# Performance work log

Measured on AMD Instinct MI355X. Metric: run time of the kernel, lower is better.

The kernel has to match this reference:

```python
import jax, jax.numpy as jnp
import numpy as np
import math

B, N, D = 4, 16384, 256
M, H = 64, 8
HD = D // H

def setup_inputs() -> dict:
    key = jax.random.key(0)
    ks = jax.random.split(key, 5)
    s = 1.0 / math.sqrt(D)
    return {
        "x": jax.random.normal(ks[0], (B, N, D), dtype=jnp.float32),
        "Ws": jax.random.normal(ks[1], (M, D), dtype=jnp.float32) * s,
        "bs": jnp.zeros((M,), dtype=jnp.float32),
        "Wqkv": jax.random.normal(ks[2], (3 * D, D), dtype=jnp.float32) * s,
        "Wo": jax.random.normal(ks[3], (D, D), dtype=jnp.float32) * s,
        "bo": jnp.zeros((D,), dtype=jnp.float32),
    }

def reference(x, Ws, bs, Wqkv, Wo, bo):
    # slice weights: softmax over N (dim=1), matching the torch code exactly
    logits = jnp.einsum('bnd,md->bnm', x, Ws) + bs          # [B,N,M]
    weights = jax.nn.softmax(logits, axis=1)                # softmax over N
    # pooling: tokens[b,m,d] = sum_n w[b,n,m] * x[b,n,d]
    tokens = jnp.einsum('bnm,bnd->bmd', weights, x)         # [B,M,D]
    # qkv projection (no bias)
    qkv = jnp.einsum('bmd,ed->bme', tokens, Wqkv)           # [B,M,3D]
    qkv = qkv.reshape(B, M, 3, H, HD)
    q = qkv[:, :, 0].transpose(0, 2, 1, 3)                  # [B,H,M,HD]
    k = qkv[:, :, 1].transpose(0, 2, 1, 3)
    v = qkv[:, :, 2].transpose(0, 2, 1, 3)
    scale = 1.0 / math.sqrt(HD)
    attn = jax.nn.softmax(jnp.einsum('bhmd,bhkd->bhmk', q, k) * scale, axis=-1)
    token_out = jnp.einsum('bhmk,bhkd->bhmd', attn, v)      # [B,H,M,HD]
    token_out = token_out.transpose(0, 2, 1, 3).reshape(B, M, D)
    token_out = jnp.einsum('bmd,ed->bme', token_out, Wo) + bo
    # unpooling: out[b,n,d] = sum_m w[b,n,m] * token_out[b,m,d]
    out = jnp.einsum('bnm,bmd->bnd', weights, token_out)    # [B,N,D]
    return out
```

## Files before the change

### kernel.cpp

```cpp
#include <hip/hip_runtime.h>
#include <math.h>

constexpr int B = 4;
constexpr int N = 16384;
constexpr int D = 256;
constexpr int M = 64;
constexpr int H = 8;

typedef __attribute__((ext_vector_type(8))) short short8;
typedef __attribute__((ext_vector_type(4))) float floatx4;

__device__ __forceinline__ float4 ld4(const float* p) {
  return *reinterpret_cast<const float4*>(p);
}
__device__ __forceinline__ void st4(float* p, float a, float b, float c, float d) {
  *reinterpret_cast<float4*>(p) = make_float4(a, b, c, d);
}
__device__ __forceinline__ unsigned short f2bf(float f) {
  unsigned u = __float_as_uint(f);
  unsigned r = (u + 0x7fffu + ((u >> 16) & 1u)) >> 16;
  return (unsigned short)r;
}

#define FMA16(acc, a4, b4)                       \
  do {                                           \
    acc[0][0] = fmaf(a4.x, b4.x, acc[0][0]);     \
    acc[0][1] = fmaf(a4.x, b4.y, acc[0][1]);     \
    acc[0][2] = fmaf(a4.x, b4.z, acc[0][2]);     \
    acc[0][3] = fmaf(a4.x, b4.w, acc[0][3]);     \
    acc[1][0] = fmaf(a4.y, b4.x, acc[1][0]);     \
    acc[1][1] = fmaf(a4.y, b4.y, acc[1][1]);     \
    acc[1][2] = fmaf(a4.y, b4.z, acc[1][2]);     \
    acc[1][3] = fmaf(a4.y, b4.w, acc[1][3]);     \
    acc[2][0] = fmaf(a4.z, b4.x, acc[2][0]);     \
    acc[2][1] = fmaf(a4.z, b4.y, acc[2][1]);     \
    acc[2][2] = fmaf(a4.z, b4.z, acc[2][2]);     \
    acc[2][3] = fmaf(a4.z, b4.w, acc[2][3]);     \
    acc[3][0] = fmaf(a4.w, b4.x, acc[3][0]);     \
    acc[3][1] = fmaf(a4.w, b4.y, acc[3][1]);     \
    acc[3][2] = fmaf(a4.w, b4.z, acc[3][2]);     \
    acc[3][3] = fmaf(a4.w, b4.w, acc[3][3]);     \
  } while (0)

__global__ __launch_bounds__(256) void k1_fused(
    const float* __restrict__ x, const float* __restrict__ Ws,
    const float* __restrict__ bs, unsigned short* __restrict__ xbT,
    unsigned short* __restrict__ En, unsigned short* __restrict__ Et,
    float* __restrict__ denom) {
  __shared__ unsigned short Xt[64][264];
  __shared__ unsigned short Wt[64][264];
  __shared__ unsigned short Es[64][72];
  __shared__ float red[64];
  const int b = blockIdx.y;
  const int n0 = blockIdx.x * 64;
  const int tid = threadIdx.x;
  const int w = tid >> 6, l = tid & 63;

#pragma unroll
  for (int p = 0; p < 16; ++p) {
    const int i = p * 256 + tid;
    const int row = i >> 6;
    const int c4 = (i & 63) * 4;
    float4 v = ld4(&x[((size_t)(b * N + n0 + row)) * D + c4]);
    unsigned u0 = (unsigned)f2bf(v.x) | ((unsigned)f2bf(v.y) << 16);
    unsigned u1 = (unsigned)f2bf(v.z) | ((unsigned)f2bf(v.w) << 16);
    *reinterpret_cast<uint2*>(&Xt[row][c4]) = make_uint2(u0, u1);
    float4 wv = ld4(&Ws[(size_t)row * D + c4]);
    unsigned w0 = (unsigned)f2bf(wv.x) | ((unsigned)f2bf(wv.y) << 16);
    unsigned w1 = (unsigned)f2bf(wv.z) | ((unsigned)f2bf(wv.w) << 16);
    *reinterpret_cast<uint2*>(&Wt[row][c4]) = make_uint2(w0, w1);
  }
  if (tid < 64) red[tid] = 0.0f;
  __syncthreads();

  floatx4 acc[4] = {{0.f, 0.f, 0.f, 0.f},
                    {0.f, 0.f, 0.f, 0.f},
                    {0.f, 0.f, 0.f, 0.f},
                    {0.f, 0.f, 0.f, 0.f}};
  const int ar = w * 16 + (l & 15);
  const int q8 = (l >> 4) * 8;
#pragma unroll
  for (int ks = 0; ks < 8; ++ks) {
    short8 a = *reinterpret_cast<short8*>(&Xt[ar][ks * 32 + q8]);
#pragma unroll
    for (int mt = 0; mt < 4; ++mt) {
      short8 bf = *reinterpret_cast<short8*>(&Wt[mt * 16 + (l & 15)][ks * 32 + q8]);
      acc[mt] = __builtin_amdgcn_mfma_f32_16x16x32_bf16(a, bf, acc[mt], 0, 0, 0);
    }
  }

  {
    const int t = tid;
#pragma unroll
    for (int g = 0; g < 4; ++g) {
      unsigned dw[8];
#pragma unroll
      for (int j = 0; j < 8; ++j) {
        const unsigned lo = Xt[g * 16 + 2 * j][t];
        const unsigned hi = Xt[g * 16 + 2 * j + 1][t];
        dw[j] = lo | (hi << 16);
      }
      const size_t base = ((size_t)(b * D + t)) * N + n0 + g * 16;
      *reinterpret_cast<uint4*>(&xbT[base]) =
          make_uint4(dw[0], dw[1], dw[2], dw[3]);
      *reinterpret_cast<uint4*>(&xbT[base + 8]) =
          make_uint4(dw[4], dw[5], dw[6], dw[7]);
    }
  }

#pragma unroll
  for (int mt = 0; mt < 4; ++mt) {
    const int m = mt * 16 + (l & 15);
    const float bsm = bs[m];
    float s = 0.0f;
#pragma unroll
    for (int r = 0; r < 4; ++r) {
      const int n = w * 16 + (l >> 4) * 4 + r;
      const float e = expf(acc[mt][r] + bsm);
      s += e;
      Es[n][m] = f2bf(e);
    }
    atomicAdd(&red[m], s);
  }
  __syncthreads();
  if (tid < 64) atomicAdd(&denom[b * M + tid], red[tid]);
#pragma unroll
  for (int p = 0; p < 2; ++p) {
    const int g = p * 256 + tid;
    const int n = g >> 3;
    const int m0 = (g & 7) * 8;
    short8 v = *reinterpret_cast<short8*>(&Es[n][m0]);
    *reinterpret_cast<short8*>(&En[((size_t)(b * N + n0 + n)) * M + m0]) = v;
  }
#pragma unroll
  for (int p = 0; p < 2; ++p) {
    const int g = p * 256 + tid;
    const int m = g >> 3;
    const int n8 = (g & 7) * 8;
    unsigned short bu[8];
#pragma unroll
    for (int k = 0; k < 8; ++k) bu[k] = Es[n8 + k][m];
    uint4 pk;
    pk.x = (unsigned)bu[0] | ((unsigned)bu[1] << 16);
    pk.y = (unsigned)bu[2] | ((unsigned)bu[3] << 16);
    pk.z = (unsigned)bu[4] | ((unsigned)bu[5] << 16);
    pk.w = (unsigned)bu[6] | ((unsigned)bu[7] << 16);
    *reinterpret_cast<uint4*>(&Et[((size_t)(b * M + m)) * N + n0 + n8]) = pk;
  }
}

__global__ __launch_bounds__(256) void k2_pool(
    const unsigned short* __restrict__ Et, const unsigned short* __restrict__ xbT,
    float* __restrict__ tokens) {
  __shared__ unsigned short EtS[64][72];
  __shared__ unsigned short XtS[64][72];
  const int dt = blockIdx.x, nc = blockIdx.y, b = blockIdx.z;
  const int d0 = dt * 64;
  const int tid = threadIdx.x;
  const int w = tid >> 6, l = tid & 63;
  floatx4 acc[4] = {{0.f, 0.f, 0.f, 0.f},
                    {0.f, 0.f, 0.f, 0.f},
                    {0.f, 0.f, 0.f, 0.f},
                    {0.f, 0.f, 0.f, 0.f}};
  const int q8 = (l >> 4) * 8;
  for (int kc = 0; kc < 8; ++kc) {
    const int nb = nc * 512 + kc * 64;
    __syncthreads();
#pragma unroll
    for (int p = 0; p < 2; ++p) {
      const int g = p * 256 + tid;
      const int row = g >> 3;
      const int c8 = (g & 7) * 8;
      *reinterpret_cast<short8*>(&EtS[row][c8]) =
          *reinterpret_cast<const short8*>(
              &Et[((size_t)(b * M + row)) * N + nb + c8]);
      *reinterpret_cast<short8*>(&XtS[row][c8]) =
          *reinterpret_cast<const short8*>(
              &xbT[((size_t)(b * D + d0 + row)) * N + nb + c8]);
    }
    __syncthreads();
#pragma unroll
    for (int ks = 0; ks < 2; ++ks) {
      short8 a = *reinterpret_cast<short8*>(&EtS[w * 16 + (l & 15)][ks * 32 + q8]);
#pragma unroll
      for (int dtile = 0; dtile < 4; ++dtile) {
        short8 bf = *reinterpret_cast<short8*>(
            &XtS[dtile * 16 + (l & 15)][ks * 32 + q8]);
        acc[dtile] =
            __builtin_amdgcn_mfma_f32_16x16x32_bf16(a, bf, acc[dtile], 0, 0, 0);
      }
    }
  }
#pragma unroll
  for (int dtile = 0; dtile < 4; ++dtile)
#pragma unroll
    for (int r = 0; r < 4; ++r) {
      const int m = w * 16 + (l >> 4) * 4 + r;
      const int d = d0 + dtile * 16 + (l & 15);
      atomicAdd(&tokens[((size_t)(b * M + m)) * D + d], acc[dtile][r]);
    }
}

__global__ __launch_bounds__(256) void k_proj(
    const float* __restrict__ A, const float* __restrict__ W,
    const float* __restrict__ bias, const float* __restrict__ denom,
    float* __restrict__ OutF, unsigned short* __restrict__ OutT, const int EC,
    const int mode) {
  __shared__ unsigned short At[64][264];
  __shared__ unsigned short Wt[64][264];
  __shared__ float Cs[64][68];
  const int et = blockIdx.x;
  const int b = blockIdx.y;
  const int tid = threadIdx.x;
  const int w = tid >> 6, l = tid & 63;
#pragma unroll
  for (int p = 0; p < 16; ++p) {
    const int i = p * 256 + tid;
    const int row = i >> 6;
    const int c4 = (i & 63) * 4;
    float4 av = ld4(&A[((size_t)(b * M + row)) * D + c4]);
    unsigned a0 = (unsigned)f2bf(av.x) | ((unsigned)f2bf(av.y) << 16);
    unsigned a1 = (unsigned)f2bf(av.z) | ((unsigned)f2bf(av.w) << 16);
    *reinterpret_cast<uint2*>(&At[row][c4]) = make_uint2(a0, a1);
    float4 wv = ld4(&W[((size_t)(et * 64 + row)) * D + c4]);
    unsigned w0 = (unsigned)f2bf(wv.x) | ((unsigned)f2bf(wv.y) << 16);
    unsigned w1 = (unsigned)f2bf(wv.z) | ((unsigned)f2bf(wv.w) << 16);
    *reinterpret_cast<uint2*>(&Wt[row][c4]) = make_uint2(w0, w1);
  }
  __syncthreads();
  floatx4 acc[4] = {{0.f, 0.f, 0.f, 0.f},
                    {0.f, 0.f, 0.f, 0.f},
                    {0.f, 0.f, 0.f, 0.f},
                    {0.f, 0.f, 0.f, 0.f}};
  const int ar = w * 16 + (l & 15);
  const int q8 = (l >> 4) * 8;
#pragma unroll
  for (int ks = 0; ks < 8; ++ks) {
    short8 a = *reinterpret_cast<short8*>(&At[ar][ks * 32 + q8]);
#pragma unroll
    for (int mt = 0; mt < 4; ++mt) {
      short8 bf = *reinterpret_cast<short8*>(&Wt[mt * 16 + (l & 15)][ks * 32 + q8]);
      acc[mt] = __builtin_amdgcn_mfma_f32_16x16x32_bf16(a, bf, acc[mt], 0, 0, 0);
    }
  }
  if (mode == 0) {
#pragma unroll
    for (int mt = 0; mt < 4; ++mt) {
#pragma unroll
      for (int r = 0; r < 4; ++r) {
        const int row = w * 16 + (l >> 4) * 4 + r;
        const float rcp = 1.0f / denom[b * M + row];
        const int e = et * 64 + mt * 16 + (l & 15);
        OutF[((size_t)(b * M + row)) * EC + e] = acc[mt][r] * rcp;
      }
    }
  } else {
#pragma unroll
    for (int mt = 0; mt < 4; ++mt) {
#pragma unroll
      for (int r = 0; r < 4; ++r) {
        const int row = w * 16 + (l >> 4) * 4 + r;
        const float rcp = 1.0f / denom[b * M + row];
        const int el = mt * 16 + (l & 15);
        const float bv = bias[et * 64 + el];
        Cs[row][el] = (acc[mt][r] + bv) * rcp;
      }
    }
    __syncthreads();
#pragma unroll
    for (int p = 0; p < 2; ++p) {
      const int g = p * 256 + tid;
      const int e = g >> 3;
      const int m0 = (g & 7) * 8;
      unsigned short bu[8];
#pragma unroll
      for (int k = 0; k < 8; ++k) bu[k] = f2bf(Cs[m0 + k][e]);
      uint4 pk;
      pk.x = (unsigned)bu[0] | ((unsigned)bu[1] << 16);
      pk.y = (unsigned)bu[2] | ((unsigned)bu[3] << 16);
      pk.z = (unsigned)bu[4] | ((unsigned)bu[5] << 16);
      pk.w = (unsigned)bu[6] | ((unsigned)bu[7] << 16);
      *reinterpret_cast<uint4*>(
          &OutT[((size_t)(b * D + et * 64 + e)) * M + m0]) = pk;
    }
  }
}

__global__ __launch_bounds__(256) void k4_attn(
    const float* __restrict__ qkv, float* __restrict__ attn_o) {
  __shared__ float qt[32][68];
  __shared__ float kt[32][68];
  __shared__ float vv[64][36];
  __shared__ float P[64][68];
  const int b = blockIdx.x >> 3;
  const int h = blockIdx.x & 7;
  const int tid = threadIdx.x;
  for (int i = tid; i < 512; i += 256) {
    const int m = i >> 3;
    const int c4 = (i & 7) * 4;
    const float* base = &qkv[((size_t)(b * M + m)) * 768 + h * 32 + c4];
    float4 q4 = ld4(base);
    float4 k4 = ld4(base + 256);
    float4 v4 = ld4(base + 512);
    qt[c4 + 0][m] = q4.x; qt[c4 + 1][m] = q4.y; qt[c4 + 2][m] = q4.z; qt[c4 + 3][m] = q4.w;
    kt[c4 + 0][m] = k4.x; kt[c4 + 1][m] = k4.y; kt[c4 + 2][m] = k4.z; kt[c4 + 3][m] = k4.w;
    *reinterpret_cast<float4*>(&vv[m][c4]) = v4;
  }
  __syncthreads();
  {
    const int tm4 = (tid & 15) * 4;
    const int tn4 = (tid >> 4) * 4;
    float acc[4][4] = {};
    for (int k = 0; k < 32; ++k) {
      float4 a4 = ld4(&qt[k][tn4]);
      float4 b4 = ld4(&kt[k][tm4]);
      FMA16(acc, a4, b4);
    }
    const float scale = 0.17677669529663687f;
#pragma unroll
    for (int i = 0; i < 4; ++i)
      st4(&P[tn4 + i][tm4], acc[i][0] * scale, acc[i][1] * scale,
          acc[i][2] * scale, acc[i][3] * scale);
  }
  __syncthreads();
  if (tid < 64) {
    float mx = -1e30f;
    for (int j = 0; j < 64; ++j) mx = fmaxf(mx, P[tid][j]);
    float s = 0.0f;
    for (int j = 0; j < 64; ++j) {
      const float e = expf(P[tid][j] - mx);
      P[tid][j] = e;
      s += e;
    }
    const float r = 1.0f / s;
    for (int j = 0; j < 64; ++j) P[tid][j] *= r;
  }
  __syncthreads();
  if (tid < 128) {
    const int i0 = (tid >> 3) * 4;
    const int c0 = (tid & 7) * 4;
    float o[4][4] = {};
    for (int j = 0; j < 64; ++j) {
      float4 v4 = ld4(&vv[j][c0]);
#pragma unroll
      for (int ii = 0; ii < 4; ++ii) {
        const float p = P[i0 + ii][j];
        o[ii][0] = fmaf(p, v4.x, o[ii][0]);
        o[ii][1] = fmaf(p, v4.y, o[ii][1]);
        o[ii][2] = fmaf(p, v4.z, o[ii][2]);
        o[ii][3] = fmaf(p, v4.w, o[ii][3]);
      }
    }
#pragma unroll
    for (int ii = 0; ii < 4; ++ii)
      st4(&attn_o[((size_t)(b * M + i0 + ii)) * D + h * 32 + c0],
          o[ii][0], o[ii][1], o[ii][2], o[ii][3]);
  }
}

__global__ __launch_bounds__(256) void k6_unpool(
    const unsigned short* __restrict__ En, const unsigned short* __restrict__ TpT,
    float* __restrict__ out) {
  __shared__ unsigned short EnS[64][72];
  __shared__ unsigned short TpS[64][72];
  const int dt = blockIdx.x, nt = blockIdx.y, b = blockIdx.z;
  const int n0 = nt * 64, d0 = dt * 64;
  const int tid = threadIdx.x;
  const int w = tid >> 6, l = tid & 63;
#pragma unroll
  for (int p = 0; p < 2; ++p) {
    const int g = p * 256 + tid;
    const int row = g >> 3;
    const int c8 = (g & 7) * 8;
    *reinterpret_cast<short8*>(&EnS[row][c8]) =
        *reinterpret_cast<const short8*>(
            &En[((size_t)(b * N + n0 + row)) * M + c8]);
    *reinterpret_cast<short8*>(&TpS[row][c8]) =
        *reinterpret_cast<const short8*>(
            &TpT[((size_t)(b * D + d0 + row)) * M + c8]);
  }
  __syncthreads();
  floatx4 acc[4] = {{0.f, 0.f, 0.f, 0.f},
                    {0.f, 0.f, 0.f, 0.f},
                    {0.f, 0.f, 0.f, 0.f},
                    {0.f, 0.f, 0.f, 0.f}};
  const int q8 = (l >> 4) * 8;
#pragma unroll
  for (int ks = 0; ks < 2; ++ks) {
    short8 a = *reinterpret_cast<short8*>(&EnS[w * 16 + (l & 15)][ks * 32 + q8]);
#pragma unroll
    for (int dtile = 0; dtile < 4; ++dtile) {
      short8 bf = *reinterpret_cast<short8*>(
          &TpS[dtile * 16 + (l & 15)][ks * 32 + q8]);
      acc[dtile] =
          __builtin_amdgcn_mfma_f32_16x16x32_bf16(a, bf, acc[dtile], 0, 0, 0);
    }
  }
#pragma unroll
  for (int dtile = 0; dtile < 4; ++dtile)
#pragma unroll
    for (int r = 0; r < 4; ++r) {
      const int n = n0 + w * 16 + (l >> 4) * 4 + r;
      const int d = d0 + dtile * 16 + (l & 15);
      out[((size_t)(b * N + n)) * D + d] = acc[dtile][r];
    }
}

extern "C" void kernel_launch(void* const* d_in, const int* in_sizes, int n_in,
                              void* d_out, int out_size, void* d_ws,
                              size_t ws_size, hipStream_t stream) {
  const float* x = (const float*)d_in[0];
  const float* Ws = (const float*)d_in[1];
  const float* bs = (const float*)d_in[2];
  const float* Wqkv = (const float*)d_in[3];
  const float* Wo = (const float*)d_in[4];
  const float* bo = (const float*)d_in[5];
  float* out = (float*)d_out;

  char* p = (char*)d_ws;
  unsigned short* xbT = (unsigned short*)p;      p += (size_t)B * N * D * 2;
  unsigned short* En = (unsigned short*)p;       p += (size_t)B * N * M * 2;
  unsigned short* Et = (unsigned short*)p;       p += (size_t)B * N * M * 2;
  unsigned short* TpT = (unsigned short*)p;      p += (size_t)B * D * M * 2;
  float* denom = (float*)p;                      p += (size_t)B * M * 4;
  float* tokens = (float*)p;                     p += (size_t)B * M * D * 4;
  float* qkv = (float*)p;                        p += (size_t)B * M * 3 * D * 4;
  float* attn_o = (float*)p;                     p += (size_t)B * M * D * 4;

  hipMemsetAsync(denom, 0, (size_t)B * M * sizeof(float), stream);
  hipMemsetAsync(tokens, 0, (size_t)B * M * D * sizeof(float), stream);

  k1_fused<<<dim3(N / 64, B), 256, 0, stream>>>(x, Ws, bs, xbT, En, Et, denom);
  k2_pool<<<dim3(D / 64, N / 512, B), 256, 0, stream>>>(Et, xbT, tokens);
  k_proj<<<dim3(12, B), 256, 0, stream>>>(tokens, Wqkv, nullptr, denom, qkv,
                                          nullptr, 768, 0);
  k4_attn<<<dim3(B * H), 256, 0, stream>>>(qkv, attn_o);
  k_proj<<<dim3(4, B), 256, 0, stream>>>(attn_o, Wo, bo, denom, nullptr, TpT,
                                         256, 1);
  k6_unpool<<<dim3(D / 64, N / 64, B), 256, 0, stream>>>(En, TpT, out);
}
```

Baseline: 188.9 us.

## Fuse QKV projection, attention and output projection into one per-batch kernel

Adds a prep kernel that converts Ws, Wqkv and Wo to bf16 once per call. k1 then reads the bf16 Ws straight from global memory instead of staging it in shared memory, which frees LDS and allows 3 blocks per CU. The separate QKV projection, attention and output projection kernels are replaced by one 512-thread block per batch that runs all three in shared memory with MFMA, including MFMA-based attention, and writes TpT directly. This removes launches and fp32 intermediate round-trips, but the fused stage runs only 4 blocks, so it has very little parallelism, and attention now uses bf16 inputs.

```diff
diff --git a/kernel.cpp b/kernel.cpp
--- a/kernel.cpp
+++ b/kernel.cpp
@@ -13,42 +13,42 @@
 __device__ __forceinline__ float4 ld4(const float* p) {
   return *reinterpret_cast<const float4*>(p);
 }
-__device__ __forceinline__ void st4(float* p, float a, float b, float c, float d) {
-  *reinterpret_cast<float4*>(p) = make_float4(a, b, c, d);
-}
 __device__ __forceinline__ unsigned short f2bf(float f) {
   unsigned u = __float_as_uint(f);
   unsigned r = (u + 0x7fffu + ((u >> 16) & 1u)) >> 16;
   return (unsigned short)r;
 }
 
-#define FMA16(acc, a4, b4)                       \
-  do {                                           \
-    acc[0][0] = fmaf(a4.x, b4.x, acc[0][0]);     \
-    acc[0][1] = fmaf(a4.x, b4.y, acc[0][1]);     \
-    acc[0][2] = fmaf(a4.x, b4.z, acc[0][2]);     \
-    acc[0][3] = fmaf(a4.x, b4.w, acc[0][3]);     \
-    acc[1][0] = fmaf(a4.y, b4.x, acc[1][0]);     \
-    acc[1][1] = fmaf(a4.y, b4.y, acc[1][1]);     \
-    acc[1][2] = fmaf(a4.y, b4.z, acc[1][2]);     \
-    acc[1][3] = fmaf(a4.y, b4.w, acc[1][3]);     \
-    acc[2][0] = fmaf(a4.z, b4.x, acc[2][0]);     \
-    acc[2][1] = fmaf(a4.z, b4.y, acc[2][1]);     \
-    acc[2][2] = fmaf(a4.z, b4.z, acc[2][2]);     \
-    acc[2][3] = fmaf(a4.z, b4.w, acc[2][3]);     \
-    acc[3][0] = fmaf(a4.w, b4.x, acc[3][0]);     \
-    acc[3][1] = fmaf(a4.w, b4.y, acc[3][1]);     \
-    acc[3][2] = fmaf(a4.w, b4.z, acc[3][2]);     \
-    acc[3][3] = fmaf(a4.w, b4.w, acc[3][3]);     \
-  } while (0)
-
-__global__ __launch_bounds__(256) void k1_fused(
-    const float* __restrict__ x, const float* __restrict__ Ws,
+__global__ __launch_bounds__(256) void k0_prep(
+    const float* __restrict__ Ws, const float* __restrict__ Wqkv,
+    const float* __restrict__ Wo, unsigned short* __restrict__ WsB,
+    unsigned short* __restrict__ WqkvB, unsigned short* __restrict__ WoB) {
+  const int g = blockIdx.x * 256 + threadIdx.x;
+  const float* src;
+  unsigned short* dst;
+  int off;
+  if (g < 2048) {
+    src = Ws; dst = WsB; off = g;
+  } else if (g < 26624) {
+    src = Wqkv; dst = WqkvB; off = g - 2048;
+  } else {
+    src = Wo; dst = WoB; off = g - 26624;
+  }
+  const float4 a = ld4(&src[(size_t)off * 8]);
+  const float4 c = ld4(&src[(size_t)off * 8 + 4]);
+  unsigned d0 = (unsigned)f2bf(a.x) | ((unsigned)f2bf(a.y) << 16);
+  unsigned d1 = (unsigned)f2bf(a.z) | ((unsigned)f2bf(a.w) << 16);
+  unsigned d2 = (unsigned)f2bf(c.x) | ((unsigned)f2bf(c.y) << 16);
+  unsigned d3 = (unsigned)f2bf(c.z) | ((unsigned)f2bf(c.w) << 16);
+  *reinterpret_cast<uint4*>(&dst[(size_t)off * 8]) = make_uint4(d0, d1, d2, d3);
+}
+
+__global__ __launch_bounds__(256, 3) void k1_fused(
+    const float* __restrict__ x, const unsigned short* __restrict__ WsB,
     const float* __restrict__ bs, unsigned short* __restrict__ xbT,
     unsigned short* __restrict__ En, unsigned short* __restrict__ Et,
     float* __restrict__ denom) {
   __shared__ unsigned short Xt[64][264];
-  __shared__ unsigned short Wt[64][264];
   __shared__ unsigned short Es[64][72];
   __shared__ float red[64];
   const int b = blockIdx.y;
@@ -65,10 +65,6 @@
     unsigned u0 = (unsigned)f2bf(v.x) | ((unsigned)f2bf(v.y) << 16);
     unsigned u1 = (unsigned)f2bf(v.z) | ((unsigned)f2bf(v.w) << 16);
     *reinterpret_cast<uint2*>(&Xt[row][c4]) = make_uint2(u0, u1);
-    float4 wv = ld4(&Ws[(size_t)row * D + c4]);
-    unsigned w0 = (unsigned)f2bf(wv.x) | ((unsigned)f2bf(wv.y) << 16);
-    unsigned w1 = (unsigned)f2bf(wv.z) | ((unsigned)f2bf(wv.w) << 16);
-    *reinterpret_cast<uint2*>(&Wt[row][c4]) = make_uint2(w0, w1);
   }
   if (tid < 64) red[tid] = 0.0f;
   __syncthreads();
@@ -84,7 +80,8 @@
     short8 a = *reinterpret_cast<short8*>(&Xt[ar][ks * 32 + q8]);
 #pragma unroll
     for (int mt = 0; mt < 4; ++mt) {
-      short8 bf = *reinterpret_cast<short8*>(&Wt[mt * 16 + (l & 15)][ks * 32 + q8]);
+      short8 bf = *reinterpret_cast<const short8*>(
+          &WsB[(size_t)(mt * 16 + (l & 15)) * 256 + ks * 32 + q8]);
       acc[mt] = __builtin_amdgcn_mfma_f32_16x16x32_bf16(a, bf, acc[mt], 0, 0, 0);
     }
   }
@@ -201,160 +198,217 @@
     }
 }
 
-__global__ __launch_bounds__(256) void k_proj(
-    const float* __restrict__ A, const float* __restrict__ W,
-    const float* __restrict__ bias, const float* __restrict__ denom,
-    float* __restrict__ OutF, unsigned short* __restrict__ OutT, const int EC,
-    const int mode) {
-  __shared__ unsigned short At[64][264];
-  __shared__ unsigned short Wt[64][264];
-  __shared__ float Cs[64][68];
-  const int et = blockIdx.x;
-  const int b = blockIdx.y;
+__global__ __launch_bounds__(512) void k_tokens(
+    const float* __restrict__ tokens, const unsigned short* __restrict__ WqkvB,
+    const unsigned short* __restrict__ WoB, const float* __restrict__ bo,
+    const float* __restrict__ denom, unsigned short* __restrict__ TpT) {
+  __shared__ __align__(16) char smem[119040];
+  unsigned short* const Tt = reinterpret_cast<unsigned short*>(smem);
+  float* const denomS = reinterpret_cast<float*>(smem + 118784);
+  const int b = blockIdx.x;
   const int tid = threadIdx.x;
-  const int w = tid >> 6, l = tid & 63;
-#pragma unroll
-  for (int p = 0; p < 16; ++p) {
-    const int i = p * 256 + tid;
+  const int w = tid >> 6;
+  const int l = tid & 63;
+  const int l15 = l & 15;
+  const int q8 = (l >> 4) * 8;
+  const int r4 = (l >> 4) * 4;
+
+#pragma unroll
+  for (int p = 0; p < 8; ++p) {
+    const int i = p * 512 + tid;
     const int row = i >> 6;
     const int c4 = (i & 63) * 4;
-    float4 av = ld4(&A[((size_t)(b * M + row)) * D + c4]);
-    unsigned a0 = (unsigned)f2bf(av.x) | ((unsigned)f2bf(av.y) << 16);
-    unsigned a1 = (unsigned)f2bf(av.z) | ((unsigned)f2bf(av.w) << 16);
-    *reinterpret_cast<uint2*>(&At[row][c4]) = make_uint2(a0, a1);
-    float4 wv = ld4(&W[((size_t)(et * 64 + row)) * D + c4]);
-    unsigned w0 = (unsigned)f2bf(wv.x) | ((unsigned)f2bf(wv.y) << 16);
-    unsigned w1 = (unsigned)f2bf(wv.z) | ((unsigned)f2bf(wv.w) << 16);
-    *reinterpret_cast<uint2*>(&Wt[row][c4]) = make_uint2(w0, w1);
-  }
-  __syncthreads();
-  floatx4 acc[4] = {{0.f, 0.f, 0.f, 0.f},
-                    {0.f, 0.f, 0.f, 0.f},
-                    {0.f, 0.f, 0.f, 0.f},
-                    {0.f, 0.f, 0.f, 0.f}};
-  const int ar = w * 16 + (l & 15);
-  const int q8 = (l >> 4) * 8;
+    float4 v = ld4(&tokens[((size_t)(b * M + row)) * D + c4]);
+    unsigned u0 = (unsigned)f2bf(v.x) | ((unsigned)f2bf(v.y) << 16);
+    unsigned u1 = (unsigned)f2bf(v.z) | ((unsigned)f2bf(v.w) << 16);
+    *reinterpret_cast<uint2*>(&Tt[row * 264 + c4]) = make_uint2(u0, u1);
+  }
+  if (tid < 64) denomS[tid] = denom[b * M + tid];
+  __syncthreads();
+
+  floatx4 acc[4][6];
+#pragma unroll
+  for (int mt = 0; mt < 4; ++mt)
+#pragma unroll
+    for (int et = 0; et < 6; ++et) acc[mt][et] = {0.f, 0.f, 0.f, 0.f};
 #pragma unroll
   for (int ks = 0; ks < 8; ++ks) {
-    short8 a = *reinterpret_cast<short8*>(&At[ar][ks * 32 + q8]);
+    short8 bfr[6];
+#pragma unroll
+    for (int et = 0; et < 6; ++et) {
+      const int e = (et >> 1) * 256 + w * 32 + (et & 1) * 16 + l15;
+      bfr[et] = *reinterpret_cast<const short8*>(
+          &WqkvB[(size_t)e * 256 + ks * 32 + q8]);
+    }
 #pragma unroll
     for (int mt = 0; mt < 4; ++mt) {
-      short8 bf = *reinterpret_cast<short8*>(&Wt[mt * 16 + (l & 15)][ks * 32 + q8]);
-      acc[mt] = __builtin_amdgcn_mfma_f32_16x16x32_bf16(a, bf, acc[mt], 0, 0, 0);
-    }
-  }
-  if (mode == 0) {
+      short8 a = *reinterpret_cast<const short8*>(
+          &Tt[(mt * 16 + l15) * 264 + ks * 32 + q8]);
+#pragma unroll
+      for (int et = 0; et < 6; ++et)
+        acc[mt][et] = __builtin_amdgcn_mfma_f32_16x16x32_bf16(a, bfr[et],
+                                                              acc[mt][et], 0, 0, 0);
+    }
+  }
+
+  float rcpd[4][4];
+#pragma unroll
+  for (int mt = 0; mt < 4; ++mt)
+#pragma unroll
+    for (int r = 0; r < 4; ++r) rcpd[mt][r] = 1.0f / denomS[mt * 16 + r4 + r];
+
+  __syncthreads();
+
+  unsigned short* const qh = reinterpret_cast<unsigned short*>(smem + w * 14848);
+  unsigned short* const kh = qh + 64 * 40;
+  unsigned short* const vT = kh + 64 * 40;
+  unsigned short* const Pp = qh;
+
+#pragma unroll
+  for (int mt = 0; mt < 4; ++mt)
+#pragma unroll
+    for (int r = 0; r < 4; ++r) {
+      const int m = mt * 16 + r4 + r;
+      const float rc = rcpd[mt][r];
+#pragma unroll
+      for (int et = 0; et < 6; ++et) {
+        const int c = (et & 1) * 16 + l15;
+        const unsigned short bv = f2bf(acc[mt][et][r] * rc);
+        if (et < 2) qh[m * 40 + c] = bv;
+        else if (et < 4) kh[m * 40 + c] = bv;
+        else vT[c * 72 + m] = bv;
+      }
+    }
+
+  short8 qf[4], kf[4];
+#pragma unroll
+  for (int t = 0; t < 4; ++t) {
+    qf[t] = *reinterpret_cast<const short8*>(&qh[(t * 16 + l15) * 40 + q8]);
+    kf[t] = *reinterpret_cast<const short8*>(&kh[(t * 16 + l15) * 40 + q8]);
+  }
+  floatx4 sa[4][4];
+#pragma unroll
+  for (int it = 0; it < 4; ++it)
+#pragma unroll
+    for (int jt = 0; jt < 4; ++jt) sa[it][jt] = {0.f, 0.f, 0.f, 0.f};
+#pragma unroll
+  for (int it = 0; it < 4; ++it)
+#pragma unroll
+    for (int jt = 0; jt < 4; ++jt)
+      sa[it][jt] =
+          __builtin_amdgcn_mfma_f32_16x16x32_bf16(qf[it], kf[jt], sa[it][jt], 0, 0, 0);
+
+  constexpr float scale = 0.17677669529663687f;
+#pragma unroll
+  for (int it = 0; it < 4; ++it)
+#pragma unroll
+    for (int r = 0; r < 4; ++r) {
+      float s0 = sa[it][0][r] * scale;
+      float s1 = sa[it][1][r] * scale;
+      float s2 = sa[it][2][r] * scale;
+      float s3 = sa[it][3][r] * scale;
+      float mx = fmaxf(fmaxf(s0, s1), fmaxf(s2, s3));
+#pragma unroll
+      for (int dd = 1; dd < 16; dd <<= 1) mx = fmaxf(mx, __shfl_xor(mx, dd));
+      const float e0 = expf(s0 - mx), e1 = expf(s1 - mx);
+      const float e2 = expf(s2 - mx), e3 = expf(s3 - mx);
+      float sm = (e0 + e1) + (e2 + e3);
+#pragma unroll
+      for (int dd = 1; dd < 16; dd <<= 1) sm += __shfl_xor(sm, dd);
+      const float ri = 1.0f / sm;
+      const int m = it * 16 + r4 + r;
+      Pp[m * 72 + l15] = f2bf(e0 * ri);
+      Pp[m * 72 + 16 + l15] = f2bf(e1 * ri);
+      Pp[m * 72 + 32 + l15] = f2bf(e2 * ri);
+      Pp[m * 72 + 48 + l15] = f2bf(e3 * ri);
+    }
+
+  floatx4 oa[4][2];
+#pragma unroll
+  for (int mt = 0; mt < 4; ++mt)
+#pragma unroll
+    for (int ht = 0; ht < 2; ++ht) oa[mt][ht] = {0.f, 0.f, 0.f, 0.f};
+#pragma unroll
+  for (int ks = 0; ks < 2; ++ks) {
+    short8 pf[4], vf[2];
+#pragma unroll
+    for (int t = 0; t < 4; ++t)
+      pf[t] = *reinterpret_cast<const short8*>(&Pp[(t * 16 + l15) * 72 + ks * 32 + q8]);
+#pragma unroll
+    for (int t = 0; t < 2; ++t)
+      vf[t] = *reinterpret_cast<const short8*>(&vT[(t * 16 + l15) * 72 + ks * 32 + q8]);
+#pragma unroll
+    for (int mt = 0; mt < 4; ++mt)
+#pragma unroll
+      for (int ht = 0; ht < 2; ++ht)
+        oa[mt][ht] =
+            __builtin_amdgcn_mfma_f32_16x16x32_bf16(pf[mt], vf[ht], oa[mt][ht], 0, 0, 0);
+  }
+  __syncthreads();
+
+  unsigned short* const Ao = reinterpret_cast<unsigned short*>(smem);
+#pragma unroll
+  for (int mt = 0; mt < 4; ++mt)
+#pragma unroll
+    for (int ht = 0; ht < 2; ++ht)
+#pragma unroll
+      for (int r = 0; r < 4; ++r)
+        Ao[(mt * 16 + r4 + r) * 264 + w * 32 + ht * 16 + l15] = f2bf(oa[mt][ht][r]);
+  __syncthreads();
+
+  floatx4 ca[4][2];
+#pragma unroll
+  for (int mt = 0; mt < 4; ++mt)
+#pragma unroll
+    for (int dt = 0; dt < 2; ++dt) ca[mt][dt] = {0.f, 0.f, 0.f, 0.f};
+#pragma unroll
+  for (int ks = 0; ks < 8; ++ks) {
+    short8 bfr2[2];
+#pragma unroll
+    for (int dt = 0; dt < 2; ++dt)
+      bfr2[dt] = *reinterpret_cast<const short8*>(
+          &WoB[(size_t)(w * 32 + dt * 16 + l15) * 256 + ks * 32 + q8]);
 #pragma unroll
     for (int mt = 0; mt < 4; ++mt) {
-#pragma unroll
-      for (int r = 0; r < 4; ++r) {
-        const int row = w * 16 + (l >> 4) * 4 + r;
-        const float rcp = 1.0f / denom[b * M + row];
-        const int e = et * 64 + mt * 16 + (l & 15);
-        OutF[((size_t)(b * M + row)) * EC + e] = acc[mt][r] * rcp;
+      short8 a = *reinterpret_cast<const short8*>(
+          &Ao[(mt * 16 + l15) * 264 + ks * 32 + q8]);
+#pragma unroll
+      for (int dt = 0; dt < 2; ++dt)
+        ca[mt][dt] =
+            __builtin_amdgcn_mfma_f32_16x16x32_bf16(a, bfr2[dt], ca[mt][dt], 0, 0, 0);
+    }
+  }
+  unsigned short* const Cs =
+      reinterpret_cast<unsigned short*>(smem + 33792 + w * 4352);
+#pragma unroll
+  for (int mt = 0; mt < 4; ++mt)
+#pragma unroll
+    for (int r = 0; r < 4; ++r) {
+      const int m = mt * 16 + r4 + r;
+      const float rc = rcpd[mt][r];
+#pragma unroll
+      for (int dt = 0; dt < 2; ++dt) {
+        const int dl = dt * 16 + l15;
+        Cs[m * 34 + dl] = f2bf((ca[mt][dt][r] + bo[w * 32 + dl]) * rc);
       }
     }
-  } else {
-#pragma unroll
-    for (int mt = 0; mt < 4; ++mt) {
-#pragma unroll
-      for (int r = 0; r < 4; ++r) {
-        const int row = w * 16 + (l >> 4) * 4 + r;
-        const float rcp = 1.0f / denom[b * M + row];
-        const int el = mt * 16 + (l & 15);
-        const float bv = bias[et * 64 + el];
-        Cs[row][el] = (acc[mt][r] + bv) * rcp;
-      }
-    }
-    __syncthreads();
-#pragma unroll
-    for (int p = 0; p < 2; ++p) {
-      const int g = p * 256 + tid;
-      const int e = g >> 3;
-      const int m0 = (g & 7) * 8;
-      unsigned short bu[8];
-#pragma unroll
-      for (int k = 0; k < 8; ++k) bu[k] = f2bf(Cs[m0 + k][e]);
-      uint4 pk;
-      pk.x = (unsigned)bu[0] | ((unsigned)bu[1] << 16);
-      pk.y = (unsigned)bu[2] | ((unsigned)bu[3] << 16);
-      pk.z = (unsigned)bu[4] | ((unsigned)bu[5] << 16);
-      pk.w = (unsigned)bu[6] | ((unsigned)bu[7] << 16);
-      *reinterpret_cast<uint4*>(
-          &OutT[((size_t)(b * D + et * 64 + e)) * M + m0]) = pk;
-    }
-  }
-}
-
-__global__ __launch_bounds__(256) void k4_attn(
-    const float* __restrict__ qkv, float* __restrict__ attn_o) {
-  __shared__ float qt[32][68];
-  __shared__ float kt[32][68];
-  __shared__ float vv[64][36];
-  __shared__ float P[64][68];
-  const int b = blockIdx.x >> 3;
-  const int h = blockIdx.x & 7;
-  const int tid = threadIdx.x;
-  for (int i = tid; i < 512; i += 256) {
-    const int m = i >> 3;
-    const int c4 = (i & 7) * 4;
-    const float* base = &qkv[((size_t)(b * M + m)) * 768 + h * 32 + c4];
-    float4 q4 = ld4(base);
-    float4 k4 = ld4(base + 256);
-    float4 v4 = ld4(base + 512);
-    qt[c4 + 0][m] = q4.x; qt[c4 + 1][m] = q4.y; qt[c4 + 2][m] = q4.z; qt[c4 + 3][m] = q4.w;
-    kt[c4 + 0][m] = k4.x; kt[c4 + 1][m] = k4.y; kt[c4 + 2][m] = k4.z; kt[c4 + 3][m] = k4.w;
-    *reinterpret_cast<float4*>(&vv[m][c4]) = v4;
-  }
-  __syncthreads();
   {
-    const int tm4 = (tid & 15) * 4;
-    const int tn4 = (tid >> 4) * 4;
-    float acc[4][4] = {};
-    for (int k = 0; k < 32; ++k) {
-      float4 a4 = ld4(&qt[k][tn4]);
-      float4 b4 = ld4(&kt[k][tm4]);
-      FMA16(acc, a4, b4);
-    }
-    const float scale = 0.17677669529663687f;
-#pragma unroll
-    for (int i = 0; i < 4; ++i)
-      st4(&P[tn4 + i][tm4], acc[i][0] * scale, acc[i][1] * scale,
-          acc[i][2] * scale, acc[i][3] * scale);
-  }
-  __syncthreads();
-  if (tid < 64) {
-    float mx = -1e30f;
-    for (int j = 0; j < 64; ++j) mx = fmaxf(mx, P[tid][j]);
-    float s = 0.0f;
-    for (int j = 0; j < 64; ++j) {
-      const float e = expf(P[tid][j] - mx);
-      P[tid][j] = e;
-      s += e;
-    }
-    const float r = 1.0f / s;
-    for (int j = 0; j < 64; ++j) P[tid][j] *= r;
-  }
-  __syncthreads();
-  if (tid < 128) {
-    const int i0 = (tid >> 3) * 4;
-    const int c0 = (tid & 7) * 4;
-    float o[4][4] = {};
-    for (int j = 0; j < 64; ++j) {
-      float4 v4 = ld4(&vv[j][c0]);
-#pragma unroll
-      for (int ii = 0; ii < 4; ++ii) {
-        const float p = P[i0 + ii][j];
-        o[ii][0] = fmaf(p, v4.x, o[ii][0]);
-        o[ii][1] = fmaf(p, v4.y, o[ii][1]);
-        o[ii][2] = fmaf(p, v4.z, o[ii][2]);
-        o[ii][3] = fmaf(p, v4.w, o[ii][3]);
-      }
-    }
-#pragma unroll
-    for (int ii = 0; ii < 4; ++ii)
-      st4(&attn_o[((size_t)(b * M + i0 + ii)) * D + h * 32 + c0],
-          o[ii][0], o[ii][1], o[ii][2], o[ii][3]);
+    const int dl = l & 31;
+    const int m0 = (l >> 5) * 32;
+    unsigned dwv[16];
+#pragma unroll
+    for (int k = 0; k < 16; ++k) {
+      const unsigned lo = Cs[(m0 + 2 * k) * 34 + dl];
+      const unsigned hi = Cs[(m0 + 2 * k + 1) * 34 + dl];
+      dwv[k] = lo | (hi << 16);
+    }
+    const size_t gb = ((size_t)(b * D + w * 32 + dl)) * M + m0;
+    *reinterpret_cast<uint4*>(&TpT[gb]) = make_uint4(dwv[0], dwv[1], dwv[2], dwv[3]);
+    *reinterpret_cast<uint4*>(&TpT[gb + 8]) = make_uint4(dwv[4], dwv[5], dwv[6], dwv[7]);
+    *reinterpret_cast<uint4*>(&TpT[gb + 16]) =
+        make_uint4(dwv[8], dwv[9], dwv[10], dwv[11]);
+    *reinterpret_cast<uint4*>(&TpT[gb + 24]) =
+        make_uint4(dwv[12], dwv[13], dwv[14], dwv[15]);
   }
 }
 
@@ -418,24 +472,22 @@
   float* out = (float*)d_out;
 
   char* p = (char*)d_ws;
-  unsigned short* xbT = (unsigned short*)p;      p += (size_t)B * N * D * 2;
-  unsigned short* En = (unsigned short*)p;       p += (size_t)B * N * M * 2;
-  unsigned short* Et = (unsigned short*)p;       p += (size_t)B * N * M * 2;
-  unsigned short* TpT = (unsigned short*)p;      p += (size_t)B * D * M * 2;
-  float* denom = (float*)p;                      p += (size_t)B * M * 4;
-  float* tokens = (float*)p;                     p += (size_t)B * M * D * 4;
-  float* qkv = (float*)p;                        p += (size_t)B * M * 3 * D * 4;
-  float* attn_o = (float*)p;                     p += (size_t)B * M * D * 4;
+  unsigned short* xbT = (unsigned short*)p;   p += (size_t)B * N * D * 2;
+  unsigned short* En = (unsigned short*)p;    p += (size_t)B * N * M * 2;
+  unsigned short* Et = (unsigned short*)p;    p += (size_t)B * N * M * 2;
+  unsigned short* TpT = (unsigned short*)p;   p += (size_t)B * D * M * 2;
+  float* denom = (float*)p;                   p += (size_t)B * M * 4;
+  float* tokens = (float*)p;                  p += (size_t)B * M * D * 4;
+  unsigned short* WsB = (unsigned short*)p;   p += (size_t)M * D * 2;
+  unsigned short* WqkvB = (unsigned short*)p; p += (size_t)3 * D * D * 2;
+  unsigned short* WoB = (unsigned short*)p;   p += (size_t)D * D * 2;
 
   hipMemsetAsync(denom, 0, (size_t)B * M * sizeof(float), stream);
   hipMemsetAsync(tokens, 0, (size_t)B * M * D * sizeof(float), stream);
 
-  k1_fused<<<dim3(N / 64, B), 256, 0, stream>>>(x, Ws, bs, xbT, En, Et, denom);
+  k0_prep<<<dim3(136), 256, 0, stream>>>(Ws, Wqkv, Wo, WsB, WqkvB, WoB);
+  k1_fused<<<dim3(N / 64, B), 256, 0, stream>>>(x, WsB, bs, xbT, En, Et, denom);
   k2_pool<<<dim3(D / 64, N / 512, B), 256, 0, stream>>>(Et, xbT, tokens);
-  k_proj<<<dim3(12, B), 256, 0, stream>>>(tokens, Wqkv, nullptr, denom, qkv,
-                                          nullptr, 768, 0);
-  k4_attn<<<dim3(B * H), 256, 0, stream>>>(qkv, attn_o);
-  k_proj<<<dim3(4, B), 256, 0, stream>>>(attn_o, Wo, bo, denom, nullptr, TpT,
-                                         256, 1);
+  k_tokens<<<dim3(B), 512, 0, stream>>>(tokens, WqkvB, WoB, bo, denom, TpT);
   k6_unpool<<<dim3(D / 64, N / 64, B), 256, 0, stream>>>(En, TpT, out);
 }
```

Measured after the change: 209.4 us. 10.9% more time.

## Drop transposed bf16 copies of x and E; pool directly from fp32 x

Applied to the files above, without the earlier changes.

k1 no longer writes the transposed bf16 copy of x or the transposed E matrix. It loads x rows straight into registers as MFMA A-fragments and reads pre-converted bf16 Ws from a new weight-prep kernel. k2 now reads fp32 x and the row-major En directly, converts x to bf16 in shared memory, and gathers the transposed MFMA fragments with scalar LDS reads. This removes about 40MB of intermediate writes and reads. The cost is a second full fp32 read of x in k2, plus strided 2-byte LDS gathers that may cause bank conflicts.

```diff
diff --git a/kernel.cpp b/kernel.cpp
--- a/kernel.cpp
+++ b/kernel.cpp
@@ -13,41 +13,40 @@
 __device__ __forceinline__ float4 ld4(const float* p) {
   return *reinterpret_cast<const float4*>(p);
 }
-__device__ __forceinline__ void st4(float* p, float a, float b, float c, float d) {
-  *reinterpret_cast<float4*>(p) = make_float4(a, b, c, d);
-}
 __device__ __forceinline__ unsigned short f2bf(float f) {
   unsigned u = __float_as_uint(f);
   unsigned r = (u + 0x7fffu + ((u >> 16) & 1u)) >> 16;
   return (unsigned short)r;
 }
 
-#define FMA16(acc, a4, b4)                       \
-  do {                                           \
-    acc[0][0] = fmaf(a4.x, b4.x, acc[0][0]);     \
-    acc[0][1] = fmaf(a4.x, b4.y, acc[0][1]);     \
-    acc[0][2] = fmaf(a4.x, b4.z, acc[0][2]);     \
-    acc[0][3] = fmaf(a4.x, b4.w, acc[0][3]);     \
-    acc[1][0] = fmaf(a4.y, b4.x, acc[1][0]);     \
-    acc[1][1] = fmaf(a4.y, b4.y, acc[1][1]);     \
-    acc[1][2] = fmaf(a4.y, b4.z, acc[1][2]);     \
-    acc[1][3] = fmaf(a4.y, b4.w, acc[1][3]);     \
-    acc[2][0] = fmaf(a4.z, b4.x, acc[2][0]);     \
-    acc[2][1] = fmaf(a4.z, b4.y, acc[2][1]);     \
-    acc[2][2] = fmaf(a4.z, b4.z, acc[2][2]);     \
-    acc[2][3] = fmaf(a4.z, b4.w, acc[2][3]);     \
-    acc[3][0] = fmaf(a4.w, b4.x, acc[3][0]);     \
-    acc[3][1] = fmaf(a4.w, b4.y, acc[3][1]);     \
-    acc[3][2] = fmaf(a4.w, b4.z, acc[3][2]);     \
-    acc[3][3] = fmaf(a4.w, b4.w, acc[3][3]);     \
-  } while (0)
-
-__global__ __launch_bounds__(256) void k1_fused(
-    const float* __restrict__ x, const float* __restrict__ Ws,
-    const float* __restrict__ bs, unsigned short* __restrict__ xbT,
-    unsigned short* __restrict__ En, unsigned short* __restrict__ Et,
+__global__ __launch_bounds__(256) void k0_prep(
+    const float* __restrict__ Ws, const float* __restrict__ Wqkv,
+    const float* __restrict__ Wo, unsigned short* __restrict__ WsB,
+    unsigned short* __restrict__ WqkvB, unsigned short* __restrict__ WoB) {
+  const int g = blockIdx.x * 256 + threadIdx.x;
+  const float* src;
+  unsigned short* dst;
+  int off;
+  if (g < 2048) {
+    src = Ws; dst = WsB; off = g;
+  } else if (g < 26624) {
+    src = Wqkv; dst = WqkvB; off = g - 2048;
+  } else {
+    src = Wo; dst = WoB; off = g - 26624;
+  }
+  const float4 a = ld4(&src[(size_t)off * 8]);
+  const float4 c = ld4(&src[(size_t)off * 8 + 4]);
+  unsigned d0 = (unsigned)f2bf(a.x) | ((unsigned)f2bf(a.y) << 16);
+  unsigned d1 = (unsigned)f2bf(a.z) | ((unsigned)f2bf(a.w) << 16);
+  unsigned d2 = (unsigned)f2bf(c.x) | ((unsigned)f2bf(c.y) << 16);
+  unsigned d3 = (unsigned)f2bf(c.z) | ((unsigned)f2bf(c.w) << 16);
+  *reinterpret_cast<uint4*>(&dst[(size_t)off * 8]) = make_uint4(d0, d1, d2, d3);
+}
+
+__global__ __launch_bounds__(256, 3) void k1_fused(
+    const float* __restrict__ x, const unsigned short* __restrict__ WsB,
+    const float* __restrict__ bs, unsigned short* __restrict__ En,
     float* __restrict__ denom) {
-  __shared__ unsigned short Xt[64][264];
   __shared__ unsigned short Wt[64][264];
   __shared__ unsigned short Es[64][72];
   __shared__ float red[64];
@@ -55,62 +54,56 @@
   const int n0 = blockIdx.x * 64;
   const int tid = threadIdx.x;
   const int w = tid >> 6, l = tid & 63;
-
-#pragma unroll
-  for (int p = 0; p < 16; ++p) {
-    const int i = p * 256 + tid;
-    const int row = i >> 6;
-    const int c4 = (i & 63) * 4;
-    float4 v = ld4(&x[((size_t)(b * N + n0 + row)) * D + c4]);
-    unsigned u0 = (unsigned)f2bf(v.x) | ((unsigned)f2bf(v.y) << 16);
-    unsigned u1 = (unsigned)f2bf(v.z) | ((unsigned)f2bf(v.w) << 16);
-    *reinterpret_cast<uint2*>(&Xt[row][c4]) = make_uint2(u0, u1);
-    float4 wv = ld4(&Ws[(size_t)row * D + c4]);
-    unsigned w0 = (unsigned)f2bf(wv.x) | ((unsigned)f2bf(wv.y) << 16);
-    unsigned w1 = (unsigned)f2bf(wv.z) | ((unsigned)f2bf(wv.w) << 16);
-    *reinterpret_cast<uint2*>(&Wt[row][c4]) = make_uint2(w0, w1);
+  const int l15 = l & 15;
+  const int q8 = (l >> 4) * 8;
+  const int ar = w * 16 + l15;
+
+  float4 fx[16];
+  const float* xrow = &x[((size_t)(b * N + n0 + ar)) * D];
+#pragma unroll
+  for (int ks = 0; ks < 8; ++ks) {
+    fx[2 * ks] = ld4(&xrow[ks * 32 + q8]);
+    fx[2 * ks + 1] = ld4(&xrow[ks * 32 + q8 + 4]);
+  }
+#pragma unroll
+  for (int p = 0; p < 8; ++p) {
+    const int u = p * 256 + tid;
+    const int row = u >> 5;
+    const int c = (u & 31) * 8;
+    *reinterpret_cast<short8*>(&Wt[row][c]) =
+        *reinterpret_cast<const short8*>(&WsB[(size_t)row * 256 + c]);
   }
   if (tid < 64) red[tid] = 0.0f;
   __syncthreads();
 
+  short8 afr[8];
+#pragma unroll
+  for (int ks = 0; ks < 8; ++ks) {
+    const float4 a0 = fx[2 * ks], a1 = fx[2 * ks + 1];
+    short8 t;
+    t[0] = (short)f2bf(a0.x); t[1] = (short)f2bf(a0.y);
+    t[2] = (short)f2bf(a0.z); t[3] = (short)f2bf(a0.w);
+    t[4] = (short)f2bf(a1.x); t[5] = (short)f2bf(a1.y);
+    t[6] = (short)f2bf(a1.z); t[7] = (short)f2bf(a1.w);
+    afr[ks] = t;
+  }
+
   floatx4 acc[4] = {{0.f, 0.f, 0.f, 0.f},
                     {0.f, 0.f, 0.f, 0.f},
                     {0.f, 0.f, 0.f, 0.f},
                     {0.f, 0.f, 0.f, 0.f}};
-  const int ar = w * 16 + (l & 15);
-  const int q8 = (l >> 4) * 8;
 #pragma unroll
   for (int ks = 0; ks < 8; ++ks) {
-    short8 a = *reinterpret_cast<short8*>(&Xt[ar][ks * 32 + q8]);
 #pragma unroll
     for (int mt = 0; mt < 4; ++mt) {
-      short8 bf = *reinterpret_cast<short8*>(&Wt[mt * 16 + (l & 15)][ks * 32 + q8]);
-      acc[mt] = __builtin_amdgcn_mfma_f32_16x16x32_bf16(a, bf, acc[mt], 0, 0, 0);
-    }
-  }
-
-  {
-    const int t = tid;
-#pragma unroll
-    for (int g = 0; g < 4; ++g) {
-      unsigned dw[8];
-#pragma unroll
-      for (int j = 0; j < 8; ++j) {
-        const unsigned lo = Xt[g * 16 + 2 * j][t];
-        const unsigned hi = Xt[g * 16 + 2 * j + 1][t];
-        dw[j] = lo | (hi << 16);
-      }
-      const size_t base = ((size_t)(b * D + t)) * N + n0 + g * 16;
-      *reinterpret_cast<uint4*>(&xbT[base]) =
-          make_uint4(dw[0], dw[1], dw[2], dw[3]);
-      *reinterpret_cast<uint4*>(&xbT[base + 8]) =
-          make_uint4(dw[4], dw[5], dw[6], dw[7]);
+      short8 bf = *reinterpret_cast<short8*>(&Wt[mt * 16 + l15][ks * 32 + q8]);
+      acc[mt] = __builtin_amdgcn_mfma_f32_16x16x32_bf16(afr[ks], bf, acc[mt], 0, 0, 0);
     }
   }
 
 #pragma unroll
   for (int mt = 0; mt < 4; ++mt) {
-    const int m = mt * 16 + (l & 15);
+    const int m = mt * 16 + l15;
     const float bsm = bs[m];
     float s = 0.0f;
 #pragma unroll
@@ -132,60 +125,62 @@
     short8 v = *reinterpret_cast<short8*>(&Es[n][m0]);
     *reinterpret_cast<short8*>(&En[((size_t)(b * N + n0 + n)) * M + m0]) = v;
   }
-#pragma unroll
-  for (int p = 0; p < 2; ++p) {
-    const int g = p * 256 + tid;
-    const int m = g >> 3;
-    const int n8 = (g & 7) * 8;
-    unsigned short bu[8];
-#pragma unroll
-    for (int k = 0; k < 8; ++k) bu[k] = Es[n8 + k][m];
-    uint4 pk;
-    pk.x = (unsigned)bu[0] | ((unsigned)bu[1] << 16);
-    pk.y = (unsigned)bu[2] | ((unsigned)bu[3] << 16);
-    pk.z = (unsigned)bu[4] | ((unsigned)bu[5] << 16);
-    pk.w = (unsigned)bu[6] | ((unsigned)bu[7] << 16);
-    *reinterpret_cast<uint4*>(&Et[((size_t)(b * M + m)) * N + n0 + n8]) = pk;
-  }
 }
 
 __global__ __launch_bounds__(256) void k2_pool(
-    const unsigned short* __restrict__ Et, const unsigned short* __restrict__ xbT,
+    const unsigned short* __restrict__ En, const float* __restrict__ x,
     float* __restrict__ tokens) {
-  __shared__ unsigned short EtS[64][72];
-  __shared__ unsigned short XtS[64][72];
+  __shared__ unsigned short Ens[64][66];
+  __shared__ unsigned short Xs[64][66];
   const int dt = blockIdx.x, nc = blockIdx.y, b = blockIdx.z;
   const int d0 = dt * 64;
   const int tid = threadIdx.x;
   const int w = tid >> 6, l = tid & 63;
+  const int l15 = l & 15;
+  const int q8 = (l >> 4) * 8;
   floatx4 acc[4] = {{0.f, 0.f, 0.f, 0.f},
                     {0.f, 0.f, 0.f, 0.f},
                     {0.f, 0.f, 0.f, 0.f},
                     {0.f, 0.f, 0.f, 0.f}};
-  const int q8 = (l >> 4) * 8;
   for (int kc = 0; kc < 8; ++kc) {
     const int nb = nc * 512 + kc * 64;
     __syncthreads();
 #pragma unroll
     for (int p = 0; p < 2; ++p) {
-      const int g = p * 256 + tid;
-      const int row = g >> 3;
-      const int c8 = (g & 7) * 8;
-      *reinterpret_cast<short8*>(&EtS[row][c8]) =
-          *reinterpret_cast<const short8*>(
-              &Et[((size_t)(b * M + row)) * N + nb + c8]);
-      *reinterpret_cast<short8*>(&XtS[row][c8]) =
-          *reinterpret_cast<const short8*>(
-              &xbT[((size_t)(b * D + d0 + row)) * N + nb + c8]);
+      const int u = p * 256 + tid;
+      const int n = u >> 3;
+      const int c8 = (u & 7) * 8;
+      short8 v = *reinterpret_cast<const short8*>(
+          &En[((size_t)(b * N + nb + n)) * M + c8]);
+      uint4 uv = *reinterpret_cast<uint4*>(&v);
+      unsigned* dp = reinterpret_cast<unsigned*>(&Ens[n][c8]);
+      dp[0] = uv.x; dp[1] = uv.y; dp[2] = uv.z; dp[3] = uv.w;
+    }
+    {
+      const int n = tid >> 2;
+      const int c16 = (tid & 3) * 16;
+      const float* xp = &x[((size_t)(b * N + nb + n)) * D + d0 + c16];
+#pragma unroll
+      for (int q = 0; q < 4; ++q) {
+        float4 v = ld4(xp + q * 4);
+        unsigned u0 = (unsigned)f2bf(v.x) | ((unsigned)f2bf(v.y) << 16);
+        unsigned u1 = (unsigned)f2bf(v.z) | ((unsigned)f2bf(v.w) << 16);
+        unsigned* dp = reinterpret_cast<unsigned*>(&Xs[n][c16 + q * 4]);
+        dp[0] = u0; dp[1] = u1;
+      }
     }
     __syncthreads();
 #pragma unroll
     for (int ks = 0; ks < 2; ++ks) {
-      short8 a = *reinterpret_cast<short8*>(&EtS[w * 16 + (l & 15)][ks * 32 + q8]);
+      const int nf = ks * 32 + q8;
+      short8 a;
+#pragma unroll
+      for (int j = 0; j < 8; ++j) a[j] = (short)Ens[nf + j][w * 16 + l15];
 #pragma unroll
       for (int dtile = 0; dtile < 4; ++dtile) {
-        short8 bf = *reinterpret_cast<short8*>(
-            &XtS[dtile * 16 + (l & 15)][ks * 32 + q8]);
+        short8 bf;
+#pragma unroll
+        for (int j = 0; j < 8; ++j) bf[j] = (short)Xs[nf + j][dtile * 16 + l15];
         acc[dtile] =
             __builtin_amdgcn_mfma_f32_16x16x32_bf16(a, bf, acc[dtile], 0, 0, 0);
       }
@@ -202,7 +197,7 @@
 }
 
 __global__ __launch_bounds__(256) void k_proj(
-    const float* __restrict__ A, const float* __restrict__ W,
+    const float* __restrict__ A, const unsigned short* __restrict__ WB,
     const float* __restrict__ bias, const float* __restrict__ denom,
     float* __restrict__ OutF, unsigned short* __restrict__ OutT, const int EC,
     const int mode) {
@@ -222,10 +217,14 @@
     unsigned a0 = (unsigned)f2bf(av.x) | ((unsigned)f2bf(av.y) << 16);
     unsigned a1 = (unsigned)f2bf(av.z) | ((unsigned)f2bf(av.w) << 16);
     *reinterpret_cast<uint2*>(&At[row][c4]) = make_uint2(a0, a1);
-    float4 wv = ld4(&W[((size_t)(et * 64 + row)) * D + c4]);
-    unsigned w0 = (unsigned)f2bf(wv.x) | ((unsigned)f2bf(wv.y) << 16);
-    unsigned w1 = (unsigned)f2bf(wv.z) | ((unsigned)f2bf(wv.w) << 16);
-    *reinterpret_cast<uint2*>(&Wt[row][c4]) = make_uint2(w0, w1);
+  }
+#pragma unroll
+  for (int p = 0; p < 8; ++p) {
+    const int u = p * 256 + tid;
+    const int row = u >> 5;
+    const int c = (u & 31) * 8;
+    *reinterpret_cast<short8*>(&Wt[row][c]) =
+        *reinterpret_cast<const short8*>(&WB[((size_t)(et * 64 + row)) * 256 + c]);
   }
   __syncthreads();
   floatx4 acc[4] = {{0.f, 0.f, 0.f, 0.f},
@@ -314,13 +313,21 @@
     for (int k = 0; k < 32; ++k) {
       float4 a4 = ld4(&qt[k][tn4]);
       float4 b4 = ld4(&kt[k][tm4]);
-      FMA16(acc, a4, b4);
+#pragma unroll
+      for (int i = 0; i < 4; ++i) {
+        const float av = (i == 0) ? a4.x : (i == 1) ? a4.y : (i == 2) ? a4.z : a4.w;
+        acc[i][0] = fmaf(av, b4.x, acc[i][0]);
+        acc[i][1] = fmaf(av, b4.y, acc[i][1]);
+        acc[i][2] = fmaf(av, b4.z, acc[i][2]);
+        acc[i][3] = fmaf(av, b4.w, acc[i][3]);
+      }
     }
     const float scale = 0.17677669529663687f;
 #pragma unroll
     for (int i = 0; i < 4; ++i)
-      st4(&P[tn4 + i][tm4], acc[i][0] * scale, acc[i][1] * scale,
-          acc[i][2] * scale, acc[i][3] * scale);
+      *reinterpret_cast<float4*>(&P[tn4 + i][tm4]) =
+          make_float4(acc[i][0] * scale, acc[i][1] * scale, acc[i][2] * scale,
+                      acc[i][3] * scale);
   }
   __syncthreads();
   if (tid < 64) {
@@ -353,8 +360,9 @@
     }
 #pragma unroll
     for (int ii = 0; ii < 4; ++ii)
-      st4(&attn_o[((size_t)(b * M + i0 + ii)) * D + h * 32 + c0],
-          o[ii][0], o[ii][1], o[ii][2], o[ii][3]);
+      *reinterpret_cast<float4*>(
+          &attn_o[((size_t)(b * M + i0 + ii)) * D + h * 32 + c0]) =
+          make_float4(o[ii][0], o[ii][1], o[ii][2], o[ii][3]);
   }
 }
 
@@ -418,24 +426,26 @@
   float* out = (float*)d_out;
 
   char* p = (char*)d_ws;
-  unsigned short* xbT = (unsigned short*)p;      p += (size_t)B * N * D * 2;
-  unsigned short* En = (unsigned short*)p;       p += (size_t)B * N * M * 2;
-  unsigned short* Et = (unsigned short*)p;       p += (size_t)B * N * M * 2;
-  unsigned short* TpT = (unsigned short*)p;      p += (size_t)B * D * M * 2;
-  float* denom = (float*)p;                      p += (size_t)B * M * 4;
-  float* tokens = (float*)p;                     p += (size_t)B * M * D * 4;
-  float* qkv = (float*)p;                        p += (size_t)B * M * 3 * D * 4;
-  float* attn_o = (float*)p;                     p += (size_t)B * M * D * 4;
+  unsigned short* En = (unsigned short*)p;    p += (size_t)B * N * M * 2;
+  unsigned short* TpT = (unsigned short*)p;   p += (size_t)B * D * M * 2;
+  float* denom = (float*)p;                   p += (size_t)B * M * 4;
+  float* tokens = (float*)p;                  p += (size_t)B * M * D * 4;
+  float* qkv = (float*)p;                     p += (size_t)B * M * 3 * D * 4;
+  float* attn_o = (float*)p;                  p += (size_t)B * M * D * 4;
+  unsigned short* WsB = (unsigned short*)p;   p += (size_t)M * D * 2;
+  unsigned short* WqkvB = (unsigned short*)p; p += (size_t)3 * D * D * 2;
+  unsigned short* WoB = (unsigned short*)p;   p += (size_t)D * D * 2;
 
   hipMemsetAsync(denom, 0, (size_t)B * M * sizeof(float), stream);
   hipMemsetAsync(tokens, 0, (size_t)B * M * D * sizeof(float), stream);
 
-  k1_fused<<<dim3(N / 64, B), 256, 0, stream>>>(x, Ws, bs, xbT, En, Et, denom);
-  k2_pool<<<dim3(D / 64, N / 512, B), 256, 0, stream>>>(Et, xbT, tokens);
-  k_proj<<<dim3(12, B), 256, 0, stream>>>(tokens, Wqkv, nullptr, denom, qkv,
+  k0_prep<<<dim3(136), 256, 0, stream>>>(Ws, Wqkv, Wo, WsB, WqkvB, WoB);
+  k1_fused<<<dim3(N / 64, B), 256, 0, stream>>>(x, WsB, bs, En, denom);
+  k2_pool<<<dim3(D / 64, N / 512, B), 256, 0, stream>>>(En, x, tokens);
+  k_proj<<<dim3(12, B), 256, 0, stream>>>(tokens, WqkvB, nullptr, denom, qkv,
                                           nullptr, 768, 0);
   k4_attn<<<dim3(B * H), 256, 0, stream>>>(qkv, attn_o);
-  k_proj<<<dim3(4, B), 256, 0, stream>>>(attn_o, Wo, bo, denom, nullptr, TpT,
+  k_proj<<<dim3(4, B), 256, 0, stream>>>(attn_o, WoB, bo, denom, nullptr, TpT,
                                          256, 1);
   k6_unpool<<<dim3(D / 64, N / 64, B), 256, 0, stream>>>(En, TpT, out);
 }
```

After: 185.8 us. No clear change (-1.6%).
